# Kernel tuning notes

Measured on AMD Instinct MI355X. Metric: run time of the kernel, lower is better.

Reference implementation:

```python
import jax, jax.numpy as jnp
import numpy as np

HEAD_SIZE = 64
D_MODEL = 1024


def setup_inputs() -> dict:
    key = jax.random.key(0)
    ks = jax.random.split(key, 6)
    B, S, D, H = 4, 4096, D_MODEL, HEAD_SIZE
    q = jax.random.normal(ks[0], (B, S, D), dtype=jnp.float32)
    k = jax.random.normal(ks[1], (B, S, D), dtype=jnp.float32)
    v = jax.random.normal(ks[2], (B, S, D), dtype=jnp.float32)
    # Linear(d_model, head_size, bias=False): stored as [D, H] so x @ W
    scale = 1.0 / np.sqrt(D)
    w_q = jax.random.normal(ks[3], (D, H), dtype=jnp.float32) * scale
    w_k = jax.random.normal(ks[4], (D, H), dtype=jnp.float32) * scale
    w_v = jax.random.normal(ks[5], (D, H), dtype=jnp.float32) * scale
    return {"q": q, "k": k, "v": v, "w_q": w_q, "w_k": w_k, "w_v": w_v}


def reference(q, k, v, w_q, w_k, w_v):
    # project: [B,S,D] @ [D,H] -> [B,S,H]
    qh = q @ w_q
    kh = k @ w_k
    vh = v @ w_v
    H = qh.shape[-1]
    # scores [B,S,S], scaled by head_size**-0.5
    rel = jnp.einsum('bqh,bkh->bqk', qh, kh) * (H ** -0.5)
    S = rel.shape[-1]
    causal = jnp.tril(jnp.ones((S, S), dtype=bool))
    rel = jnp.where(causal, rel, -jnp.inf)
    weights = jax.nn.softmax(rel, axis=-1)
    return jnp.einsum('bqk,bkh->bqh', weights, vh)
```

## Files before the change

kernel.cpp:

```cpp
#include <hip/hip_runtime.h>
#include <hip/hip_bf16.h>
#include <cstdint>

#define D_MODEL 1024
#define HEAD    64
#define SEQ     4096
#define BATCH   4
#define NROWS   (BATCH * SEQ)

typedef __attribute__((ext_vector_type(8))) short short8;
typedef __attribute__((ext_vector_type(4))) float floatx4;

__device__ __forceinline__ ushort f2bf(float f) {
    union { __hip_bfloat16 h; ushort u; } c;
    c.h = __float2bfloat16(f);
    return c.u;
}
__device__ __forceinline__ uint pk2(float a, float b) {
    return (uint)f2bf(a) | ((uint)f2bf(b) << 16);
}

__device__ __forceinline__ void gload16(const void* g, void* l) {
    __builtin_amdgcn_global_load_lds(
        (const __attribute__((address_space(1))) unsigned int*)g,
        (__attribute__((address_space(3))) unsigned int*)l, 16, 0, 0);
}

__global__ __launch_bounds__(256) void wprep_kernel(
    const float* __restrict__ wq, const float* __restrict__ wk,
    const float* __restrict__ wv, ushort* __restrict__ wt)
{
    const int which = blockIdx.y;
    const int k0    = blockIdx.x * 64;
    const float* w  = (which == 0) ? wq : (which == 1) ? wk : wv;
    const int tid   = threadIdx.x;

    __shared__ ushort lds[64][65];

#pragma unroll
    for (int i = 0; i < 16; ++i) {
        int idx = tid + 256 * i;
        int kl  = idx >> 6;
        int n   = idx & 63;
        lds[n][kl] = f2bf(w[(size_t)(k0 + kl) * 64 + n]);
    }
    __syncthreads();
#pragma unroll
    for (int i = 0; i < 16; ++i) {
        int idx = tid + 256 * i;
        int n   = idx >> 6;
        int kl  = idx & 63;
        wt[(size_t)(which * 64 + n) * D_MODEL + k0 + kl] = lds[n][kl];
    }
}

__global__ __launch_bounds__(256) void proj_kernel(
    const float* __restrict__ xq, const float* __restrict__ xk,
    const float* __restrict__ xv, const ushort* __restrict__ wt,
    ushort* __restrict__ qh, ushort* __restrict__ kh, ushort* __restrict__ vt)
{
    const int which = blockIdx.y;
    const float*  x = (which == 0) ? xq : (which == 1) ? xk : xv;
    const ushort* w = wt + (size_t)which * 64 * D_MODEL;

    const int row0 = blockIdx.x * 64;
    const int tid  = threadIdx.x;
    const int wv   = tid >> 6;
    const int ln   = tid & 63;
    const int l16  = ln & 15;
    const int quad = ln >> 4;

    __shared__ float  Abuf[2][64 * 64];
    __shared__ ushort Wbuf[2][64 * 64];

    const float* asrc[4];
#pragma unroll
    for (int i = 0; i < 4; ++i) {
        int j  = wv * 4 + i;
        int lr = 4 * j + (ln >> 4);
        int cf = ((ln & 15) ^ (lr & 15)) * 4;
        asrc[i] = x + (size_t)(row0 + lr) * D_MODEL + cf;
    }
    const ushort* wsrc[2];
#pragma unroll
    for (int i = 0; i < 2; ++i) {
        int j  = wv * 2 + i;
        int n  = 8 * j + (ln >> 3);
        int kc = ((ln & 7) ^ (ln >> 3)) * 8;
        wsrc[i] = w + (size_t)n * D_MODEL + kc;
    }

    floatx4 acc[4] = {};

#define STAGE(buf, kk)                                                        \
    do {                                                                      \
        char* ab_ = (char*)&Abuf[buf][0];                                     \
        char* wb_ = (char*)&Wbuf[buf][0];                                     \
        _Pragma("unroll")                                                     \
        for (int i_ = 0; i_ < 4; ++i_)                                        \
            gload16(asrc[i_] + (kk), ab_ + (wv * 4 + i_) * 1024);             \
        _Pragma("unroll")                                                     \
        for (int i_ = 0; i_ < 2; ++i_)                                        \
            gload16(wsrc[i_] + (kk), wb_ + (wv * 2 + i_) * 1024);             \
    } while (0)

#define COMPUTE(buf)                                                          \
    do {                                                                      \
        const char* ab_ = (const char*)&Abuf[buf][0];                         \
        const char* wb_ = (const char*)&Wbuf[buf][0];                         \
        const int arow_ = wv * 16 + l16;                                      \
        const int akey_ = l16 << 4;                         \
        _Pragma("unroll")                                                     \
        for (int ks_ = 0; ks_ < 2; ++ks_) {                                   \
            const int colb_ = (ks_ * 32 + quad * 8) * 4;                      \
            float4 f0 = *(const float4*)(ab_ + arow_ * 256 + ((colb_)      ^ akey_)); \
            float4 f1 = *(const float4*)(ab_ + arow_ * 256 + ((colb_ + 16) ^ akey_)); \
            union { short8 s; uint u[4]; } a_;                                \
            a_.u[0] = pk2(f0.x, f0.y); a_.u[1] = pk2(f0.z, f0.w);             \
            a_.u[2] = pk2(f1.x, f1.y); a_.u[3] = pk2(f1.z, f1.w);             \
            const int wcolb_ = (ks_ * 32 + quad * 8) * 2;                     \
            const int wkey_  = (l16 & 7) << 4;     \
            _Pragma("unroll")                                                 \
            for (int nt_ = 0; nt_ < 4; ++nt_) {                               \
                const int n_ = nt_ * 16 + l16;                                \
                short8 bf_ = *(const short8*)(wb_ + n_ * 128 + (wcolb_ ^ wkey_)); \
                acc[nt_] = __builtin_amdgcn_mfma_f32_16x16x32_bf16(a_.s, bf_, acc[nt_], 0, 0, 0); \
            }                                                                 \
        }                                                                     \
    } while (0)

    STAGE(0, 0);
    __syncthreads();
    for (int t = 0; t < 16; ++t) {
        if (t + 1 < 16) STAGE((t + 1) & 1, (t + 1) * 64);
        COMPUTE(t & 1);
        __syncthreads();
    }
#undef STAGE
#undef COMPUTE

    const int rbase = row0 + wv * 16 + quad * 4;
    if (which < 2) {
        ushort* y = (which == 0) ? qh : kh;
        const float sc = (which == 0) ? 0.125f : 1.0f;
#pragma unroll
        for (int nt = 0; nt < 4; ++nt) {
            int h = nt * 16 + l16;
#pragma unroll
            for (int r = 0; r < 4; ++r)
                y[(size_t)(rbase + r) * HEAD + h] = f2bf(acc[nt][r] * sc);
        }
    } else {
        const int b  = rbase >> 12;
        const int s0 = rbase & (SEQ - 1);
#pragma unroll
        for (int nt = 0; nt < 4; ++nt) {
            int h = nt * 16 + l16;
            uint2 pk = make_uint2(pk2(acc[nt][0], acc[nt][1]), pk2(acc[nt][2], acc[nt][3]));
            *(uint2*)&vt[(size_t)(b * 64 + h) * SEQ + s0] = pk;
        }
    }
}

__global__ __launch_bounds__(256, 2) void attn_kernel(
    const ushort* __restrict__ qh, const ushort* __restrict__ kh,
    const ushort* __restrict__ vt, float* __restrict__ out)
{
    const int b    = blockIdx.x >> 7;
    const int i    = blockIdx.x & 127;
    const int qsA  = i, qsB = 255 - i;
    const int q0A  = qsA * 16, q0B = qsB * 16;
    const int nA   = (qsA >> 2) + 1;
    const int nB   = (qsB >> 2) + 1;
    const int tid  = threadIdx.x;
    const int wv   = tid >> 6;
    const int ln   = tid & 63;
    const int l16  = ln & 15;
    const int quad = ln >> 4;

    __shared__ ushort PA[4][16 * 72];
    __shared__ ushort PB[4][16 * 72];
    __shared__ float  Obuf[4][16][68];
    __shared__ float  Lbuf[4][16];

    const ushort* khb = kh + (size_t)b * SEQ * HEAD;
    const ushort* vtb = vt + (size_t)b * HEAD * SEQ;

    const size_t qbA = ((size_t)b * SEQ + q0A + l16) * HEAD + quad * 8;
    const size_t qbB = ((size_t)b * SEQ + q0B + l16) * HEAD + quad * 8;
    const short8 qA0 = *(const short8*)(qh + qbA);
    const short8 qA1 = *(const short8*)(qh + qbA + 32);
    const short8 qB0 = *(const short8*)(qh + qbB);
    const short8 qB1 = *(const short8*)(qh + qbB + 32);

    floatx4 OA[4] = {}, OB[4] = {};
    float rsA = 0.f, rsB = 0.f;
    ushort* myPA = PA[wv];
    ushort* myPB = PB[wv];

    const int cA = (nA > wv) ? (((nA - 1 - wv) >> 2) + 1) : 0;
    const int cB = ((nB - 1 - wv) >> 2) + 1;
    const int steps = (cA > cB) ? cA : cB;

    for (int s = 0; s < steps; ++s) {
        const int ktA = wv + 4 * s, ktB = wv + 4 * s;
        const bool doA = s < cA, doB = s < cB;
        const int k0A = ktA * 64, k0B = ktB * 64;

        short8 kfA[8], vfA[8], kfB[8], vfB[8];
        if (doA) {
#pragma unroll
            for (int nt = 0; nt < 4; ++nt) {
                const ushort* vp = vtb + (size_t)(nt * 16 + l16) * SEQ + k0A + quad * 8;
                vfA[nt * 2] = *(const short8*)vp; vfA[nt * 2 + 1] = *(const short8*)(vp + 32);
                const ushort* kp = khb + (size_t)(k0A + nt * 16 + l16) * HEAD + quad * 8;
                kfA[nt * 2] = *(const short8*)kp; kfA[nt * 2 + 1] = *(const short8*)(kp + 32);
            }
        }
        if (doB) {
#pragma unroll
            for (int nt = 0; nt < 4; ++nt) {
                const ushort* vp = vtb + (size_t)(nt * 16 + l16) * SEQ + k0B + quad * 8;
                vfB[nt * 2] = *(const short8*)vp; vfB[nt * 2 + 1] = *(const short8*)(vp + 32);
                const ushort* kp = khb + (size_t)(k0B + nt * 16 + l16) * HEAD + quad * 8;
                kfB[nt * 2] = *(const short8*)kp; kfB[nt * 2 + 1] = *(const short8*)(kp + 32);
            }
        }

        floatx4 aA[4], aB[4];
        if (doA) {
#pragma unroll
            for (int nt = 0; nt < 4; ++nt) {
                floatx4 c = {};
                c = __builtin_amdgcn_mfma_f32_16x16x32_bf16(kfA[nt * 2],     qA0, c, 0, 0, 0);
                c = __builtin_amdgcn_mfma_f32_16x16x32_bf16(kfA[nt * 2 + 1], qA1, c, 0, 0, 0);
                aA[nt] = c;
            }
        }
        if (doB) {
#pragma unroll
            for (int nt = 0; nt < 4; ++nt) {
                floatx4 c = {};
                c = __builtin_amdgcn_mfma_f32_16x16x32_bf16(kfB[nt * 2],     qB0, c, 0, 0, 0);
                c = __builtin_amdgcn_mfma_f32_16x16x32_bf16(kfB[nt * 2 + 1], qB1, c, 0, 0, 0);
                aB[nt] = c;
            }
        }

        if (doA) {
            const bool masked = (ktA == nA - 1);
#pragma unroll
            for (int nt = 0; nt < 4; ++nt) {
                union { ushort u[4]; uint2 w; } pk;
#pragma unroll
                for (int r = 0; r < 4; ++r) {
                    float sv = aA[nt][r];
                    if (masked && (k0A + nt * 16 + quad * 4 + r > q0A + l16)) sv = -3.0e38f;
                    float p = __expf(sv);
                    rsA += p;
                    pk.u[r] = f2bf(p);
                }
                *(uint2*)&myPA[l16 * 72 + nt * 16 + quad * 4] = pk.w;
            }
        }
        if (doB) {
            const bool masked = (ktB == nB - 1);
#pragma unroll
            for (int nt = 0; nt < 4; ++nt) {
                union { ushort u[4]; uint2 w; } pk;
#pragma unroll
                for (int r = 0; r < 4; ++r) {
                    float sv = aB[nt][r];
                    if (masked && (k0B + nt * 16 + quad * 4 + r > q0B + l16)) sv = -3.0e38f;
                    float p = __expf(sv);
                    rsB += p;
                    pk.u[r] = f2bf(p);
                }
                *(uint2*)&myPB[l16 * 72 + nt * 16 + quad * 4] = pk.w;
            }
        }

        if (doA) {
            short8 p0 = *(const short8*)&myPA[l16 * 72 + quad * 8];
            short8 p1 = *(const short8*)&myPA[l16 * 72 + 32 + quad * 8];
#pragma unroll
            for (int nt = 0; nt < 4; ++nt) {
                OA[nt] = __builtin_amdgcn_mfma_f32_16x16x32_bf16(p0, vfA[nt * 2],     OA[nt], 0, 0, 0);
                OA[nt] = __builtin_amdgcn_mfma_f32_16x16x32_bf16(p1, vfA[nt * 2 + 1], OA[nt], 0, 0, 0);
            }
        }
        if (doB) {
            short8 p0 = *(const short8*)&myPB[l16 * 72 + quad * 8];
            short8 p1 = *(const short8*)&myPB[l16 * 72 + 32 + quad * 8];
#pragma unroll
            for (int nt = 0; nt < 4; ++nt) {
                OB[nt] = __builtin_amdgcn_mfma_f32_16x16x32_bf16(p0, vfB[nt * 2],     OB[nt], 0, 0, 0);
                OB[nt] = __builtin_amdgcn_mfma_f32_16x16x32_bf16(p1, vfB[nt * 2 + 1], OB[nt], 0, 0, 0);
            }
        }
    }

    rsA += __shfl_xor(rsA, 16); rsA += __shfl_xor(rsA, 32);
    if (quad == 0) Lbuf[wv][l16] = rsA;
#pragma unroll
    for (int nt = 0; nt < 4; ++nt)
#pragma unroll
        for (int r = 0; r < 4; ++r)
            Obuf[wv][quad * 4 + r][nt * 16 + l16] = OA[nt][r];
    __syncthreads();
    {
        const int row = tid >> 4, h0 = (tid & 15) * 4;
        float l = Lbuf[0][row] + Lbuf[1][row] + Lbuf[2][row] + Lbuf[3][row];
        float inv = 1.f / l;
        float4 o;
        o.x = (Obuf[0][row][h0+0] + Obuf[1][row][h0+0] + Obuf[2][row][h0+0] + Obuf[3][row][h0+0]) * inv;
        o.y = (Obuf[0][row][h0+1] + Obuf[1][row][h0+1] + Obuf[2][row][h0+1] + Obuf[3][row][h0+1]) * inv;
        o.z = (Obuf[0][row][h0+2] + Obuf[1][row][h0+2] + Obuf[2][row][h0+2] + Obuf[3][row][h0+2]) * inv;
        o.w = (Obuf[0][row][h0+3] + Obuf[1][row][h0+3] + Obuf[2][row][h0+3] + Obuf[3][row][h0+3]) * inv;
        *(float4*)&out[((size_t)b * SEQ + q0A + row) * HEAD + h0] = o;
    }
    __syncthreads();

    rsB += __shfl_xor(rsB, 16); rsB += __shfl_xor(rsB, 32);
    if (quad == 0) Lbuf[wv][l16] = rsB;
#pragma unroll
    for (int nt = 0; nt < 4; ++nt)
#pragma unroll
        for (int r = 0; r < 4; ++r)
            Obuf[wv][quad * 4 + r][nt * 16 + l16] = OB[nt][r];
    __syncthreads();
    {
        const int row = tid >> 4, h0 = (tid & 15) * 4;
        float l = Lbuf[0][row] + Lbuf[1][row] + Lbuf[2][row] + Lbuf[3][row];
        float inv = 1.f / l;
        float4 o;
        o.x = (Obuf[0][row][h0+0] + Obuf[1][row][h0+0] + Obuf[2][row][h0+0] + Obuf[3][row][h0+0]) * inv;
        o.y = (Obuf[0][row][h0+1] + Obuf[1][row][h0+1] + Obuf[2][row][h0+1] + Obuf[3][row][h0+1]) * inv;
        o.z = (Obuf[0][row][h0+2] + Obuf[1][row][h0+2] + Obuf[2][row][h0+2] + Obuf[3][row][h0+2]) * inv;
        o.w = (Obuf[0][row][h0+3] + Obuf[1][row][h0+3] + Obuf[2][row][h0+3] + Obuf[3][row][h0+3]) * inv;
        *(float4*)&out[((size_t)b * SEQ + q0B + row) * HEAD + h0] = o;
    }
}

extern "C" void kernel_launch(void* const* d_in, const int* in_sizes, int n_in,
                              void* d_out, int out_size, void* d_ws, size_t ws_size,
                              hipStream_t stream) {
    const float* q  = (const float*)d_in[0];
    const float* k  = (const float*)d_in[1];
    const float* v  = (const float*)d_in[2];
    const float* wq = (const float*)d_in[3];
    const float* wk = (const float*)d_in[4];
    const float* wv = (const float*)d_in[5];

    ushort* qh = (ushort*)d_ws;
    ushort* kh = qh + (size_t)NROWS * HEAD;
    ushort* vt = kh + (size_t)NROWS * HEAD;
    ushort* wt = vt + (size_t)NROWS * HEAD;

    dim3 wgrid(D_MODEL / 64, 3);
    wprep_kernel<<<wgrid, 256, 0, stream>>>(wq, wk, wv, wt);

    dim3 pgrid(NROWS / 64, 3);
    proj_kernel<<<pgrid, 256, 0, stream>>>(q, k, v, wt, qh, kh, vt);

    attn_kernel<<<BATCH * 128, 256, 0, stream>>>(qh, kh, vt, (float*)d_out);
}
```

Baseline: 268.7 us.

## Give each wave private LDS staging and drop block barriers in projection GEMM

The projection kernel now gives every wave its own LDS region and stages only its own 16 rows of X plus a private copy of the weight tile. It steps through K in chunks of 32 and keeps two chunks in flight, ordered with explicit vmcnt waits and scheduling barriers. This removes all __syncthreads from the K loop so waves run independently. In exchange, weight traffic is duplicated across the four waves and each chunk gets smaller, doubling the number of loop iterations.

```diff
diff --git a/kernel.cpp b/kernel.cpp
--- a/kernel.cpp
+++ b/kernel.cpp
@@ -70,73 +70,76 @@
     const int l16  = ln & 15;
     const int quad = ln >> 4;
 
-    __shared__ float  Abuf[2][64 * 64];
-    __shared__ ushort Wbuf[2][64 * 64];
-
-    const float* asrc[4];
-#pragma unroll
-    for (int i = 0; i < 4; ++i) {
-        int j  = wv * 4 + i;
-        int lr = 4 * j + (ln >> 4);
-        int cf = ((ln & 15) ^ (lr & 15)) * 4;
-        asrc[i] = x + (size_t)(row0 + lr) * D_MODEL + cf;
-    }
-    const ushort* wsrc[2];
-#pragma unroll
-    for (int i = 0; i < 2; ++i) {
-        int j  = wv * 2 + i;
-        int n  = 8 * j + (ln >> 3);
-        int kc = ((ln & 7) ^ (ln >> 3)) * 8;
-        wsrc[i] = w + (size_t)n * D_MODEL + kc;
-    }
+    __shared__ alignas(16) char lds[4][12288];
+    char* Ab = &lds[wv][0];
+    char* Wb = &lds[wv][4096];
+
+    const float* aS[2];
+#pragma unroll
+    for (int i = 0; i < 2; ++i)
+        aS[i] = x + (size_t)(row0 + wv * 16 + i * 8 + (ln >> 3)) * D_MODEL
+                  + ((ln & 7) ^ (ln >> 3)) * 4;
+    const ushort* wS[4];
+#pragma unroll
+    for (int j = 0; j < 4; ++j)
+        wS[j] = w + (size_t)(j * 16 + (ln >> 2)) * D_MODEL
+                  + (((ln & 3) ^ ((ln >> 3) & 3)) * 8);
 
     floatx4 acc[4] = {};
 
-#define STAGE(buf, kk)                                                        \
+#define ISSUE(buf, tt)                                                        \
     do {                                                                      \
-        char* ab_ = (char*)&Abuf[buf][0];                                     \
-        char* wb_ = (char*)&Wbuf[buf][0];                                     \
-        _Pragma("unroll")                                                     \
-        for (int i_ = 0; i_ < 4; ++i_)                                        \
-            gload16(asrc[i_] + (kk), ab_ + (wv * 4 + i_) * 1024);             \
-        _Pragma("unroll")                                                     \
-        for (int i_ = 0; i_ < 2; ++i_)                                        \
-            gload16(wsrc[i_] + (kk), wb_ + (wv * 2 + i_) * 1024);             \
+        __builtin_amdgcn_sched_barrier(0);                                    \
+        gload16(aS[0] + (tt) * 32, Ab + (buf) * 2048 + 0 * 1024);             \
+        gload16(aS[1] + (tt) * 32, Ab + (buf) * 2048 + 1 * 1024);             \
+        gload16(wS[0] + (tt) * 32, Wb + (buf) * 4096 + 0 * 1024);             \
+        gload16(wS[1] + (tt) * 32, Wb + (buf) * 4096 + 1 * 1024);             \
+        gload16(wS[2] + (tt) * 32, Wb + (buf) * 4096 + 2 * 1024);             \
+        gload16(wS[3] + (tt) * 32, Wb + (buf) * 4096 + 3 * 1024);             \
+        __builtin_amdgcn_sched_barrier(0);                                    \
+    } while (0)
+
+#define WAITV6                                                                \
+    do {                                                                      \
+        asm volatile("s_waitcnt vmcnt(6)" ::: "memory");                      \
+        __builtin_amdgcn_sched_barrier(0);                                    \
+    } while (0)
+#define WAITV0                                                                \
+    do {                                                                      \
+        asm volatile("s_waitcnt vmcnt(0)" ::: "memory");                      \
+        __builtin_amdgcn_sched_barrier(0);                                    \
     } while (0)
 
 #define COMPUTE(buf)                                                          \
     do {                                                                      \
-        const char* ab_ = (const char*)&Abuf[buf][0];                         \
-        const char* wb_ = (const char*)&Wbuf[buf][0];                         \
-        const int arow_ = wv * 16 + l16;                                      \
-        const int akey_ = l16 << 4;                         \
+        const char* ab_ = Ab + (buf) * 2048;                                  \
+        const char* wb_ = Wb + (buf) * 4096;                                  \
+        const int ak_ = l16 & 7;                                              \
+        float4 f0 = *(const float4*)(ab_ + l16 * 128 + (((quad * 2 + 0) ^ ak_) << 4)); \
+        float4 f1 = *(const float4*)(ab_ + l16 * 128 + (((quad * 2 + 1) ^ ak_) << 4)); \
+        union { short8 s; uint u[4]; } a_;                                    \
+        a_.u[0] = pk2(f0.x, f0.y); a_.u[1] = pk2(f0.z, f0.w);                 \
+        a_.u[2] = pk2(f1.x, f1.y); a_.u[3] = pk2(f1.z, f1.w);                 \
+        const int wk_ = (l16 >> 1) & 3;                                       \
         _Pragma("unroll")                                                     \
-        for (int ks_ = 0; ks_ < 2; ++ks_) {                                   \
-            const int colb_ = (ks_ * 32 + quad * 8) * 4;                      \
-            float4 f0 = *(const float4*)(ab_ + arow_ * 256 + ((colb_)      ^ akey_)); \
-            float4 f1 = *(const float4*)(ab_ + arow_ * 256 + ((colb_ + 16) ^ akey_)); \
-            union { short8 s; uint u[4]; } a_;                                \
-            a_.u[0] = pk2(f0.x, f0.y); a_.u[1] = pk2(f0.z, f0.w);             \
-            a_.u[2] = pk2(f1.x, f1.y); a_.u[3] = pk2(f1.z, f1.w);             \
-            const int wcolb_ = (ks_ * 32 + quad * 8) * 2;                     \
-            const int wkey_  = (l16 & 7) << 4;     \
-            _Pragma("unroll")                                                 \
-            for (int nt_ = 0; nt_ < 4; ++nt_) {                               \
-                const int n_ = nt_ * 16 + l16;                                \
-                short8 bf_ = *(const short8*)(wb_ + n_ * 128 + (wcolb_ ^ wkey_)); \
-                acc[nt_] = __builtin_amdgcn_mfma_f32_16x16x32_bf16(a_.s, bf_, acc[nt_], 0, 0, 0); \
-            }                                                                 \
+        for (int nt_ = 0; nt_ < 4; ++nt_) {                                   \
+            short8 bf_ = *(const short8*)(wb_ + (nt_ * 16 + l16) * 64 + ((quad ^ wk_) << 4)); \
+            acc[nt_] = __builtin_amdgcn_mfma_f32_16x16x32_bf16(a_.s, bf_, acc[nt_], 0, 0, 0); \
         }                                                                     \
     } while (0)
 
-    STAGE(0, 0);
-    __syncthreads();
-    for (int t = 0; t < 16; ++t) {
-        if (t + 1 < 16) STAGE((t + 1) & 1, (t + 1) * 64);
+    ISSUE(0, 0);
+    ISSUE(1, 1);
+    for (int t = 0; t < 30; ++t) {
+        WAITV6;
         COMPUTE(t & 1);
-        __syncthreads();
-    }
-#undef STAGE
+        ISSUE(t & 1, t + 2);
+    }
+    WAITV6;  COMPUTE(0);
+    WAITV0;  COMPUTE(1);
+#undef ISSUE
+#undef WAITV6
+#undef WAITV0
 #undef COMPUTE
 
     const int rbase = row0 + wv * 16 + quad * 4;
```

Result: slower. 282.9 us (+5.3%).

## Split paired query tiles into one tile per block, heaviest-first ordering

Applied to the files above, without the earlier changes.

The attention kernel no longer pairs a light and a heavy 16-row query tile in each block. It launches twice as many blocks, each handling one tile, ordered from the longest causal range down with batch varying fastest. Launch bounds rise to 3 blocks per SM. This aims to raise occupancy and cut register pressure, relying on heaviest-first scheduling for load balance. In exchange it loses the explicit pairing balance and the interleaving of two independent streams within a wave.

```diff
diff --git a/kernel.cpp b/kernel.cpp
--- a/kernel.cpp
+++ b/kernel.cpp
@@ -162,146 +162,86 @@
     }
 }
 
-__global__ __launch_bounds__(256, 2) void attn_kernel(
+__global__ __launch_bounds__(256, 3) void attn_kernel(
     const ushort* __restrict__ qh, const ushort* __restrict__ kh,
     const ushort* __restrict__ vt, float* __restrict__ out)
 {
-    const int b    = blockIdx.x >> 7;
-    const int i    = blockIdx.x & 127;
-    const int qsA  = i, qsB = 255 - i;
-    const int q0A  = qsA * 16, q0B = qsB * 16;
-    const int nA   = (qsA >> 2) + 1;
-    const int nB   = (qsB >> 2) + 1;
+    const int bid = blockIdx.x;
+    const int qs  = 255 - (bid >> 2);
+    const int b   = bid & 3;
+    const int q0  = qs * 16;
+    const int ni  = (qs >> 2) + 1;
     const int tid  = threadIdx.x;
     const int wv   = tid >> 6;
     const int ln   = tid & 63;
     const int l16  = ln & 15;
     const int quad = ln >> 4;
 
-    __shared__ ushort PA[4][16 * 72];
-    __shared__ ushort PB[4][16 * 72];
+    __shared__ ushort P[4][16 * 72];
     __shared__ float  Obuf[4][16][68];
     __shared__ float  Lbuf[4][16];
 
     const ushort* khb = kh + (size_t)b * SEQ * HEAD;
     const ushort* vtb = vt + (size_t)b * HEAD * SEQ;
 
-    const size_t qbA = ((size_t)b * SEQ + q0A + l16) * HEAD + quad * 8;
-    const size_t qbB = ((size_t)b * SEQ + q0B + l16) * HEAD + quad * 8;
-    const short8 qA0 = *(const short8*)(qh + qbA);
-    const short8 qA1 = *(const short8*)(qh + qbA + 32);
-    const short8 qB0 = *(const short8*)(qh + qbB);
-    const short8 qB1 = *(const short8*)(qh + qbB + 32);
-
-    floatx4 OA[4] = {}, OB[4] = {};
-    float rsA = 0.f, rsB = 0.f;
-    ushort* myPA = PA[wv];
-    ushort* myPB = PB[wv];
-
-    const int cA = (nA > wv) ? (((nA - 1 - wv) >> 2) + 1) : 0;
-    const int cB = ((nB - 1 - wv) >> 2) + 1;
-    const int steps = (cA > cB) ? cA : cB;
-
-    for (int s = 0; s < steps; ++s) {
-        const int ktA = wv + 4 * s, ktB = wv + 4 * s;
-        const bool doA = s < cA, doB = s < cB;
-        const int k0A = ktA * 64, k0B = ktB * 64;
-
-        short8 kfA[8], vfA[8], kfB[8], vfB[8];
-        if (doA) {
-#pragma unroll
-            for (int nt = 0; nt < 4; ++nt) {
-                const ushort* vp = vtb + (size_t)(nt * 16 + l16) * SEQ + k0A + quad * 8;
-                vfA[nt * 2] = *(const short8*)vp; vfA[nt * 2 + 1] = *(const short8*)(vp + 32);
-                const ushort* kp = khb + (size_t)(k0A + nt * 16 + l16) * HEAD + quad * 8;
-                kfA[nt * 2] = *(const short8*)kp; kfA[nt * 2 + 1] = *(const short8*)(kp + 32);
+    const size_t qb = ((size_t)b * SEQ + q0 + l16) * HEAD + quad * 8;
+    const short8 qf0 = *(const short8*)(qh + qb);
+    const short8 qf1 = *(const short8*)(qh + qb + 32);
+
+    floatx4 OA[4] = {};
+    float rs = 0.f;
+    ushort* myP = P[wv];
+
+    const int c = (ni > wv) ? (((ni - 1 - wv) >> 2) + 1) : 0;
+
+    for (int s = 0; s < c; ++s) {
+        const int kt = wv + 4 * s;
+        const int k0 = kt * 64;
+
+        short8 kf[8], vf[8];
+#pragma unroll
+        for (int nt = 0; nt < 4; ++nt) {
+            const ushort* vp = vtb + (size_t)(nt * 16 + l16) * SEQ + k0 + quad * 8;
+            vf[nt * 2] = *(const short8*)vp; vf[nt * 2 + 1] = *(const short8*)(vp + 32);
+            const ushort* kp = khb + (size_t)(k0 + nt * 16 + l16) * HEAD + quad * 8;
+            kf[nt * 2] = *(const short8*)kp; kf[nt * 2 + 1] = *(const short8*)(kp + 32);
+        }
+
+        floatx4 a[4];
+#pragma unroll
+        for (int nt = 0; nt < 4; ++nt) {
+            floatx4 cc = {};
+            cc = __builtin_amdgcn_mfma_f32_16x16x32_bf16(kf[nt * 2],     qf0, cc, 0, 0, 0);
+            cc = __builtin_amdgcn_mfma_f32_16x16x32_bf16(kf[nt * 2 + 1], qf1, cc, 0, 0, 0);
+            a[nt] = cc;
+        }
+
+        const bool masked = (kt == ni - 1);
+#pragma unroll
+        for (int nt = 0; nt < 4; ++nt) {
+            union { ushort u[4]; uint2 w; } pk;
+#pragma unroll
+            for (int r = 0; r < 4; ++r) {
+                float sv = a[nt][r];
+                if (masked && (k0 + nt * 16 + quad * 4 + r > q0 + l16)) sv = -3.0e38f;
+                float p = __expf(sv);
+                rs += p;
+                pk.u[r] = f2bf(p);
             }
-        }
-        if (doB) {
-#pragma unroll
-            for (int nt = 0; nt < 4; ++nt) {
-                const ushort* vp = vtb + (size_t)(nt * 16 + l16) * SEQ + k0B + quad * 8;
-                vfB[nt * 2] = *(const short8*)vp; vfB[nt * 2 + 1] = *(const short8*)(vp + 32);
-                const ushort* kp = khb + (size_t)(k0B + nt * 16 + l16) * HEAD + quad * 8;
-                kfB[nt * 2] = *(const short8*)kp; kfB[nt * 2 + 1] = *(const short8*)(kp + 32);
-            }
-        }
-
-        floatx4 aA[4], aB[4];
-        if (doA) {
-#pragma unroll
-            for (int nt = 0; nt < 4; ++nt) {
-                floatx4 c = {};
-                c = __builtin_amdgcn_mfma_f32_16x16x32_bf16(kfA[nt * 2],     qA0, c, 0, 0, 0);
-                c = __builtin_amdgcn_mfma_f32_16x16x32_bf16(kfA[nt * 2 + 1], qA1, c, 0, 0, 0);
-                aA[nt] = c;
-            }
-        }
-        if (doB) {
-#pragma unroll
-            for (int nt = 0; nt < 4; ++nt) {
-                floatx4 c = {};
-                c = __builtin_amdgcn_mfma_f32_16x16x32_bf16(kfB[nt * 2],     qB0, c, 0, 0, 0);
-                c = __builtin_amdgcn_mfma_f32_16x16x32_bf16(kfB[nt * 2 + 1], qB1, c, 0, 0, 0);
-                aB[nt] = c;
-            }
-        }
-
-        if (doA) {
-            const bool masked = (ktA == nA - 1);
-#pragma unroll
-            for (int nt = 0; nt < 4; ++nt) {
-                union { ushort u[4]; uint2 w; } pk;
-#pragma unroll
-                for (int r = 0; r < 4; ++r) {
-                    float sv = aA[nt][r];
-                    if (masked && (k0A + nt * 16 + quad * 4 + r > q0A + l16)) sv = -3.0e38f;
-                    float p = __expf(sv);
-                    rsA += p;
-                    pk.u[r] = f2bf(p);
-                }
-                *(uint2*)&myPA[l16 * 72 + nt * 16 + quad * 4] = pk.w;
-            }
-        }
-        if (doB) {
-            const bool masked = (ktB == nB - 1);
-#pragma unroll
-            for (int nt = 0; nt < 4; ++nt) {
-                union { ushort u[4]; uint2 w; } pk;
-#pragma unroll
-                for (int r = 0; r < 4; ++r) {
-                    float sv = aB[nt][r];
-                    if (masked && (k0B + nt * 16 + quad * 4 + r > q0B + l16)) sv = -3.0e38f;
-                    float p = __expf(sv);
-                    rsB += p;
-                    pk.u[r] = f2bf(p);
-                }
-                *(uint2*)&myPB[l16 * 72 + nt * 16 + quad * 4] = pk.w;
-            }
-        }
-
-        if (doA) {
-            short8 p0 = *(const short8*)&myPA[l16 * 72 + quad * 8];
-            short8 p1 = *(const short8*)&myPA[l16 * 72 + 32 + quad * 8];
-#pragma unroll
-            for (int nt = 0; nt < 4; ++nt) {
-                OA[nt] = __builtin_amdgcn_mfma_f32_16x16x32_bf16(p0, vfA[nt * 2],     OA[nt], 0, 0, 0);
-                OA[nt] = __builtin_amdgcn_mfma_f32_16x16x32_bf16(p1, vfA[nt * 2 + 1], OA[nt], 0, 0, 0);
-            }
-        }
-        if (doB) {
-            short8 p0 = *(const short8*)&myPB[l16 * 72 + quad * 8];
-            short8 p1 = *(const short8*)&myPB[l16 * 72 + 32 + quad * 8];
-#pragma unroll
-            for (int nt = 0; nt < 4; ++nt) {
-                OB[nt] = __builtin_amdgcn_mfma_f32_16x16x32_bf16(p0, vfB[nt * 2],     OB[nt], 0, 0, 0);
-                OB[nt] = __builtin_amdgcn_mfma_f32_16x16x32_bf16(p1, vfB[nt * 2 + 1], OB[nt], 0, 0, 0);
-            }
-        }
-    }
-
-    rsA += __shfl_xor(rsA, 16); rsA += __shfl_xor(rsA, 32);
-    if (quad == 0) Lbuf[wv][l16] = rsA;
+            *(uint2*)&myP[l16 * 72 + nt * 16 + quad * 4] = pk.w;
+        }
+
+        short8 p0 = *(const short8*)&myP[l16 * 72 + quad * 8];
+        short8 p1 = *(const short8*)&myP[l16 * 72 + 32 + quad * 8];
+#pragma unroll
+        for (int nt = 0; nt < 4; ++nt) {
+            OA[nt] = __builtin_amdgcn_mfma_f32_16x16x32_bf16(p0, vf[nt * 2],     OA[nt], 0, 0, 0);
+            OA[nt] = __builtin_amdgcn_mfma_f32_16x16x32_bf16(p1, vf[nt * 2 + 1], OA[nt], 0, 0, 0);
+        }
+    }
+
+    rs += __shfl_xor(rs, 16); rs += __shfl_xor(rs, 32);
+    if (quad == 0) Lbuf[wv][l16] = rs;
 #pragma unroll
     for (int nt = 0; nt < 4; ++nt)
 #pragma unroll
@@ -317,28 +257,7 @@
         o.y = (Obuf[0][row][h0+1] + Obuf[1][row][h0+1] + Obuf[2][row][h0+1] + Obuf[3][row][h0+1]) * inv;
         o.z = (Obuf[0][row][h0+2] + Obuf[1][row][h0+2] + Obuf[2][row][h0+2] + Obuf[3][row][h0+2]) * inv;
         o.w = (Obuf[0][row][h0+3] + Obuf[1][row][h0+3] + Obuf[2][row][h0+3] + Obuf[3][row][h0+3]) * inv;
-        *(float4*)&out[((size_t)b * SEQ + q0A + row) * HEAD + h0] = o;
-    }
-    __syncthreads();
-
-    rsB += __shfl_xor(rsB, 16); rsB += __shfl_xor(rsB, 32);
-    if (quad == 0) Lbuf[wv][l16] = rsB;
-#pragma unroll
-    for (int nt = 0; nt < 4; ++nt)
-#pragma unroll
-        for (int r = 0; r < 4; ++r)
-            Obuf[wv][quad * 4 + r][nt * 16 + l16] = OB[nt][r];
-    __syncthreads();
-    {
-        const int row = tid >> 4, h0 = (tid & 15) * 4;
-        float l = Lbuf[0][row] + Lbuf[1][row] + Lbuf[2][row] + Lbuf[3][row];
-        float inv = 1.f / l;
-        float4 o;
-        o.x = (Obuf[0][row][h0+0] + Obuf[1][row][h0+0] + Obuf[2][row][h0+0] + Obuf[3][row][h0+0]) * inv;
-        o.y = (Obuf[0][row][h0+1] + Obuf[1][row][h0+1] + Obuf[2][row][h0+1] + Obuf[3][row][h0+1]) * inv;
-        o.z = (Obuf[0][row][h0+2] + Obuf[1][row][h0+2] + Obuf[2][row][h0+2] + Obuf[3][row][h0+2]) * inv;
-        o.w = (Obuf[0][row][h0+3] + Obuf[1][row][h0+3] + Obuf[2][row][h0+3] + Obuf[3][row][h0+3]) * inv;
-        *(float4*)&out[((size_t)b * SEQ + q0B + row) * HEAD + h0] = o;
+        *(float4*)&out[((size_t)b * SEQ + q0 + row) * HEAD + h0] = o;
     }
 }
 
@@ -363,5 +282,5 @@
     dim3 pgrid(NROWS / 64, 3);
     proj_kernel<<<pgrid, 256, 0, stream>>>(q, k, v, wt, qh, kh, vt);
 
-    attn_kernel<<<BATCH * 128, 256, 0, stream>>>(qh, kh, vt, (float*)d_out);
-}
+    attn_kernel<<<BATCH * 256, 256, 0, stream>>>(qh, kh, vt, (float*)d_out);
+}
```

Result: slower. 284.0 us (+5.7%).
